# Kernel optimization log

Hardware: AMD Instinct MI355X
Metric: run time of the kernel (lower is better)

Reference implementation:

```python
import jax, jax.numpy as jnp
import numpy as np

B, T, D, H = 8, 2048, 1024, 128  # batch, seq, input_size, head_size


def setup_inputs() -> dict:
    key = jax.random.key(0)
    kx, kq, kk, kv = jax.random.split(key, 4)
    s = 1.0 / np.sqrt(D)
    return {
        "x": jax.random.normal(kx, (B, T, D), dtype=jnp.float32),
        "Wq": jax.random.normal(kq, (D, H), dtype=jnp.float32) * s,
        "Wk": jax.random.normal(kk, (D, H), dtype=jnp.float32) * s,
        "Wv": jax.random.normal(kv, (D, H), dtype=jnp.float32) * s,
    }


def reference(x, Wq, Wk, Wv):
    # projections (Linear, no bias)
    q = jnp.einsum("btd,dh->bth", x, Wq)
    k = jnp.einsum("btd,dh->bth", x, Wk)
    v = jnp.einsum("btd,dh->bth", x, Wv)
    scale = H ** (-0.5)
    scores = jnp.einsum("bth,bsh->bts", q, k) * scale  # [B,T,T]
    t = x.shape[1]
    causal = jnp.tril(jnp.ones((t, t), dtype=bool))
    scores = jnp.where(causal, scores, -jnp.inf)
    attn = jax.nn.softmax(scores, axis=-1)  # dropout p=0.0 -> identity
    out = jnp.einsum("bts,bsh->bth", attn, v)
    return out
```

## Files before the change

### kernel.cpp

```cpp
#include <hip/hip_runtime.h>
#include <math.h>

#define B_ 8
#define T_ 2048
#define D_ 1024
#define H_ 128
#define BT (B_ * T_)

typedef short bf16x8 __attribute__((ext_vector_type(8)));
typedef float f32x4 __attribute__((ext_vector_type(4)));

static constexpr float SCALE = 0.08838834764831845f;

__device__ inline unsigned short f2b(float f) {
  unsigned int u = __float_as_uint(f);
  u += 0x7FFF + ((u >> 16) & 1);
  return (unsigned short)(u >> 16);
}
__device__ inline unsigned int pk2(float a, float b) {
  return (unsigned int)f2b(a) | ((unsigned int)f2b(b) << 16);
}

__device__ __forceinline__ void gll16(const void* g, void* l) {
  __builtin_amdgcn_global_load_lds(
      (const __attribute__((address_space(1))) void*)g,
      (__attribute__((address_space(3))) void*)l, 16, 0, 0);
}

__global__ __launch_bounds__(256) void wcvt_kernel(
    const float* __restrict__ Wq, const float* __restrict__ Wk,
    const float* __restrict__ Wv, short* __restrict__ Wt) {
  __shared__ short Wls[128 * 72];
  const int sel = blockIdx.y;
  const float* W = sel == 0 ? Wq : (sel == 1 ? Wk : Wv);
  const int d0 = blockIdx.x * 64;
  const int tid = threadIdx.x;
#pragma unroll
  for (int i = 0; i < 8; ++i) {
    int slot = tid + i * 256;
    int r = slot >> 5, hg = slot & 31;
    float4 w = *(const float4*)(W + (size_t)(d0 + r) * H_ + hg * 4);
    Wls[(hg * 4 + 0) * 72 + r] = (short)f2b(w.x);
    Wls[(hg * 4 + 1) * 72 + r] = (short)f2b(w.y);
    Wls[(hg * 4 + 2) * 72 + r] = (short)f2b(w.z);
    Wls[(hg * 4 + 3) * 72 + r] = (short)f2b(w.w);
  }
  __syncthreads();
  short* dst = Wt + (size_t)sel * D_ * H_;
#pragma unroll
  for (int i = 0; i < 4; ++i) {
    int slot = tid + i * 256;
    int h = slot >> 3, g = slot & 7;
    *(int4*)(dst + (size_t)h * D_ + d0 + g * 8) = *(int4*)&Wls[h * 72 + g * 8];
  }
}

__global__ __launch_bounds__(256) void proj_kernel(
    const float* __restrict__ x, const short* __restrict__ Wt,
    short* __restrict__ qb, short* __restrict__ kb, short* __restrict__ vtb) {
  __shared__ alignas(16) char smem[49152];
  short* Xs0 = (short*)smem;
  short* Xs1 = (short*)(smem + 8192);
  short* Ws0 = (short*)(smem + 16384);
  short* Ws1 = (short*)(smem + 32768);

  const int tid = threadIdx.x;
  const int wave = tid >> 6, lane = tid & 63;
  const int ln = lane & 15, quad = lane >> 4;
  const int mw = wave & 1, nw = wave >> 1;
  const int sel = blockIdx.y;
  const int row0 = blockIdx.x * 64;
  const short* W = Wt + (size_t)sel * (size_t)(D_ * H_);

  f32x4 acc[2][4];
#pragma unroll
  for (int mi = 0; mi < 2; ++mi)
#pragma unroll
    for (int ni = 0; ni < 4; ++ni) acc[mi][ni] = (f32x4){0.f, 0.f, 0.f, 0.f};

  auto stage = [&](int bf, int k0) {
    short* Ws = bf ? Ws1 : Ws0;
#pragma unroll
    for (int j = 0; j < 4; ++j) {
      const int rbase = wave * 32 + j * 8;
      const int n = rbase + (lane >> 3);
      const int gp = (lane & 7) ^ (n & 7);
      gll16(W + (size_t)n * D_ + k0 + gp * 8, (char*)Ws + rbase * 128);
    }
    short* Xs = bf ? Xs1 : Xs0;
    float4 xr[4];
#pragma unroll
    for (int i = 0; i < 4; ++i) {
      int fid = tid + i * 256;
      int r = fid >> 4, g4 = fid & 15;
      xr[i] = *(const float4*)(x + (size_t)(row0 + r) * D_ + k0 + g4 * 4);
    }
#pragma unroll
    for (int i = 0; i < 4; ++i) {
      int fid = tid + i * 256;
      int r = fid >> 4, g4 = fid & 15;
      int g = g4 >> 1, half = g4 & 1;
      unsigned int* p = (unsigned int*)&Xs[r * 64 + ((g ^ (r & 7)) * 8) + half * 4];
      p[0] = pk2(xr[i].x, xr[i].y);
      p[1] = pk2(xr[i].z, xr[i].w);
    }
  };

  stage(0, 0);
  for (int s = 0; s < 16; ++s) {
    __syncthreads();
    if (s < 15) stage((s + 1) & 1, (s + 1) * 64);
    const short* Xs = (s & 1) ? Xs1 : Xs0;
    const short* Ws = (s & 1) ? Ws1 : Ws0;
#pragma unroll
    for (int kk = 0; kk < 2; ++kk) {
      bf16x8 a[2];
#pragma unroll
      for (int mi = 0; mi < 2; ++mi) {
        int r = mw * 32 + mi * 16 + ln;
        a[mi] = *(bf16x8*)&Xs[r * 64 + (((kk * 4 + quad) ^ (r & 7)) * 8)];
      }
#pragma unroll
      for (int ni = 0; ni < 4; ++ni) {
        int n = nw * 64 + ni * 16 + ln;
        bf16x8 bb = *(bf16x8*)&Ws[n * 64 + (((kk * 4 + quad) ^ (n & 7)) * 8)];
#pragma unroll
        for (int mi = 0; mi < 2; ++mi)
          acc[mi][ni] = __builtin_amdgcn_mfma_f32_16x16x32_bf16(a[mi], bb, acc[mi][ni], 0, 0, 0);
      }
    }
  }

  __syncthreads();
  short* Cs = (short*)smem;
  if (sel < 2) {
    short* out = sel ? kb : qb;
#pragma unroll
    for (int mi = 0; mi < 2; ++mi)
#pragma unroll
      for (int ni = 0; ni < 4; ++ni)
#pragma unroll
        for (int rr = 0; rr < 4; ++rr)
          Cs[(mw * 32 + mi * 16 + quad * 4 + rr) * 136 + nw * 64 + ni * 16 + ln] =
              (short)f2b(acc[mi][ni][rr]);
    __syncthreads();
#pragma unroll
    for (int i = 0; i < 4; ++i) {
      int slot = tid + i * 256;
      int r = slot >> 4, g = slot & 15;
      *(int4*)(out + (size_t)(row0 + r) * H_ + g * 8) = *(int4*)&Cs[r * 136 + g * 8];
    }
  } else {
#pragma unroll
    for (int mi = 0; mi < 2; ++mi)
#pragma unroll
      for (int ni = 0; ni < 4; ++ni)
#pragma unroll
        for (int rr = 0; rr < 4; ++rr)
          Cs[(nw * 64 + ni * 16 + ln) * 72 + mw * 32 + mi * 16 + quad * 4 + rr] =
              (short)f2b(acc[mi][ni][rr]);
    __syncthreads();
    const int b = row0 >> 11, t0 = row0 & 2047;
#pragma unroll
    for (int i = 0; i < 4; ++i) {
      int slot = tid + i * 256;
      int h = slot >> 3, g = slot & 7;
      *(int4*)(vtb + (size_t)(b * H_ + h) * T_ + t0 + g * 8) = *(int4*)&Cs[h * 72 + g * 8];
    }
  }
}

__global__ __launch_bounds__(256) void attn_part(
    const short* __restrict__ qb, const short* __restrict__ kb,
    const short* __restrict__ vtb, float* __restrict__ po,
    float* __restrict__ pm, float* __restrict__ pl) {
  __shared__ alignas(16) char smem[74240];
  short* Ks0 = (short*)smem;
  short* Ks1 = (short*)(smem + 16384);
  short* Vt0 = (short*)(smem + 32768);
  short* Vt1 = (short*)(smem + 49152);
  short* Pt  = (short*)(smem + 65536);

  const int tid = threadIdx.x;
  const int wv = tid >> 6, lane = tid & 63;
  const int ln = lane & 15, quad = lane >> 4;
  const int b = blockIdx.x / 80;
  const int rr = 79 - (blockIdx.x % 80);
  const int g = (rr >= 48) ? 3 : (rr >= 24) ? 2 : (rr >= 8) ? 1 : 0;
  const int local = rr - 4 * g * (g + 1);
  const int j = 8 * g + local / (g + 1);
  const int s = local - (local / (g + 1)) * (g + 1);
  const int sid = b * 80 + rr;
  const int q0 = j * 64;
  const int nchunks = min(8, j + 1 - 8 * s);

  short* myP = Pt + wv * (16 * 68);

  bf16x8 qfr[4];
#pragma unroll
  for (int kk = 0; kk < 4; ++kk)
    qfr[kk] = *(const bf16x8*)(qb + (size_t)(b * T_ + q0 + wv * 16 + ln) * H_ +
                               kk * 32 + quad * 8);

  f32x4 oacc[8];
#pragma unroll
  for (int ht = 0; ht < 8; ++ht) oacc[ht] = (f32x4){0.f, 0.f, 0.f, 0.f};

  float m_run = -INFINITY, l_run = 0.f;
  const int qglob = q0 + wv * 16 + ln;

  auto stageK = [&](short* dst, int s0) {
#pragma unroll
    for (int jj = 0; jj < 4; ++jj) {
      const int rb = wv * 16 + jj * 4;
      const int r = rb + (lane >> 4);
      const int gp = (lane & 15) ^ (r & 7);
      gll16(kb + (size_t)(b * T_ + s0 + r) * H_ + gp * 8, (char*)dst + rb * 256);
    }
  };
  auto stageV = [&](short* dst, int s0) {
#pragma unroll
    for (int jj = 0; jj < 4; ++jj) {
      const int hb = wv * 32 + jj * 8;
      const int h = hb + (lane >> 3);
      const int gp = (lane & 7) ^ (h & 7);
      gll16(vtb + (size_t)(b * H_ + h) * T_ + s0 + gp * 8, (char*)dst + hb * 128);
    }
  };

  stageK(Ks0, 8 * s * 64);
  stageV(Vt0, 8 * s * 64);

  for (int ch = 0; ch < nchunks; ++ch) {
    const int s0 = (8 * s + ch) * 64;
    const int cur = ch & 1;
    __syncthreads();
    if (ch + 1 < nchunks) {
      stageK(cur ? Ks0 : Ks1, s0 + 64);
      stageV(cur ? Vt0 : Vt1, s0 + 64);
    }
    const short* Kc = cur ? Ks1 : Ks0;
    const short* Vc = cur ? Vt1 : Vt0;

    f32x4 sacc[4];
#pragma unroll
    for (int t = 0; t < 4; ++t) sacc[t] = (f32x4){0.f, 0.f, 0.f, 0.f};
#pragma unroll
    for (int kk = 0; kk < 4; ++kk) {
#pragma unroll
      for (int t = 0; t < 4; ++t) {
        const int krow = t * 16 + ln;
        bf16x8 kf = *(bf16x8*)&Kc[krow * 128 + (((kk * 4 + quad) ^ (ln & 7)) * 8)];
        sacc[t] = __builtin_amdgcn_mfma_f32_16x16x32_bf16(kf, qfr[kk], sacc[t], 0, 0, 0);
      }
    }

    float sv[4][4];
    float mc = -INFINITY;
#pragma unroll
    for (int t = 0; t < 4; ++t)
#pragma unroll
      for (int r = 0; r < 4; ++r) {
        const int key = s0 + t * 16 + quad * 4 + r;
        float sc = sacc[t][r] * SCALE;
        sv[t][r] = (key <= qglob) ? sc : -INFINITY;
        mc = fmaxf(mc, sv[t][r]);
      }
    mc = fmaxf(mc, __shfl_xor(mc, 16));
    mc = fmaxf(mc, __shfl_xor(mc, 32));
    const float mnew = fmaxf(m_run, mc);
    const float alpha = __expf(m_run - mnew);
    float lc = 0.f;
    float p[4][4];
#pragma unroll
    for (int t = 0; t < 4; ++t)
#pragma unroll
      for (int r = 0; r < 4; ++r) {
        p[t][r] = __expf(sv[t][r] - mnew);
        lc += p[t][r];
      }
    lc += __shfl_xor(lc, 16);
    lc += __shfl_xor(lc, 32);
    l_run = l_run * alpha + lc;
    m_run = mnew;

#pragma unroll
    for (int t = 0; t < 4; ++t) {
      *(unsigned int*)&myP[ln * 68 + t * 16 + quad * 4 + 0] = pk2(p[t][0], p[t][1]);
      *(unsigned int*)&myP[ln * 68 + t * 16 + quad * 4 + 2] = pk2(p[t][2], p[t][3]);
    }
#pragma unroll
    for (int ht = 0; ht < 8; ++ht)
#pragma unroll
      for (int r = 0; r < 4; ++r) oacc[ht][r] *= alpha;

#pragma unroll
    for (int kk2 = 0; kk2 < 2; ++kk2) {
      bf16x8 pf = *(bf16x8*)&myP[ln * 68 + kk2 * 32 + quad * 8];
#pragma unroll
      for (int ht = 0; ht < 8; ++ht) {
        const int hrow = ht * 16 + ln;
        bf16x8 vf = *(bf16x8*)&Vc[hrow * 64 + (((kk2 * 4 + quad) ^ (ln & 7)) * 8)];
        oacc[ht] = __builtin_amdgcn_mfma_f32_16x16x32_bf16(vf, pf, oacc[ht], 0, 0, 0);
      }
    }
  }

  if (quad == 0) {
    pm[(size_t)sid * 64 + wv * 16 + ln] = m_run;
    pl[(size_t)sid * 64 + wv * 16 + ln] = l_run;
  }
  __syncthreads();
  float* Ot = (float*)smem;
#pragma unroll
  for (int ht = 0; ht < 8; ++ht)
    *(f32x4*)&Ot[(wv * 16 + ln) * 132 + ht * 16 + quad * 4] = oacc[ht];
  __syncthreads();
  float* dst = po + (size_t)sid * 8192;
#pragma unroll
  for (int i = 0; i < 8; ++i) {
    int slot2 = tid + i * 256;
    int r2 = slot2 >> 5, c2 = slot2 & 31;
    *(f32x4*)(dst + r2 * 128 + c2 * 4) = *(f32x4*)&Ot[r2 * 132 + c2 * 4];
  }
}

__global__ __launch_bounds__(256) void attn_reduce(
    const float* __restrict__ po, const float* __restrict__ pm,
    const float* __restrict__ pl, float* __restrict__ out) {
  const int b = blockIdx.x >> 5;
  const int j = blockIdx.x & 31;
  const int g = j >> 3;
  const int nseg = g + 1;
  const int sid0 = b * 80 + 4 * g * (g + 1) + (j - 8 * g) * nseg;
  const int tid = threadIdx.x;
  const int q = tid >> 2, hq = tid & 3;

  float m[4], l[4], a[4];
  float M = -INFINITY;
  for (int s2 = 0; s2 < nseg; ++s2) {
    m[s2] = pm[(size_t)(sid0 + s2) * 64 + q];
    l[s2] = pl[(size_t)(sid0 + s2) * 64 + q];
    M = fmaxf(M, m[s2]);
  }
  float lsum = 0.f;
  for (int s2 = 0; s2 < nseg; ++s2) {
    a[s2] = __expf(m[s2] - M);
    lsum += a[s2] * l[s2];
  }
  f32x4 acc[8];
#pragma unroll
  for (int i = 0; i < 8; ++i) acc[i] = (f32x4){0.f, 0.f, 0.f, 0.f};
  for (int s2 = 0; s2 < nseg; ++s2) {
    const float* src = po + (size_t)(sid0 + s2) * 8192 + q * 128 + hq * 32;
    const float as = a[s2];
#pragma unroll
    for (int i = 0; i < 8; ++i) {
      f32x4 v = *(const f32x4*)(src + i * 4);
#pragma unroll
      for (int c = 0; c < 4; ++c) acc[i][c] += as * v[c];
    }
  }
  const float inv = 1.0f / lsum;
  float* o = out + ((size_t)(b * T_ + j * 64 + q)) * H_ + hq * 32;
#pragma unroll
  for (int i = 0; i < 8; ++i) {
    f32x4 v;
#pragma unroll
    for (int c = 0; c < 4; ++c) v[c] = acc[i][c] * inv;
    *(f32x4*)(o + i * 4) = v;
  }
}

extern "C" void kernel_launch(void* const* d_in, const int* in_sizes, int n_in,
                              void* d_out, int out_size, void* d_ws, size_t ws_size,
                              hipStream_t stream) {
  const float* x  = (const float*)d_in[0];
  const float* Wq = (const float*)d_in[1];
  const float* Wk = (const float*)d_in[2];
  const float* Wv = (const float*)d_in[3];
  float* out = (float*)d_out;

  char* ws = (char*)d_ws;
  short* qb  = (short*)(ws);
  short* kb  = (short*)(ws + 4194304);
  short* vtb = (short*)(ws + 8388608);
  short* Wt  = (short*)(ws + 12582912);
  float* po  = (float*)(ws + 14680064);
  float* pm  = (float*)(ws + 35651584);
  float* pl  = (float*)(ws + 35915776);

  wcvt_kernel<<<dim3(D_ / 64, 3), 256, 0, stream>>>(Wq, Wk, Wv, Wt);
  proj_kernel<<<dim3(BT / 64, 3), 256, 0, stream>>>(x, Wt, qb, kb, vtb);
  attn_part<<<dim3(8 * 80), 256, 0, stream>>>(qb, kb, vtb, po, pm, pl);
  attn_reduce<<<dim3(8 * 32), 256, 0, stream>>>(po, pm, pl, out);
}
```

Before: 165.7 us.

## Enlarge attention query tile to 128 rows and overlap X loads with MFMA

The attention kernel now gives each wave 32 query rows (two 16-row sub-tiles) instead of 16. Each block covers 128 queries and the split-KV grid is halved, so each K/V chunk staged into LDS is reused twice as much. Score scaling is folded into a log2e-scaled constant so exp2f can be used, and the causal mask is applied only on chunks that cross the diagonal. The projection kernel issues the next X tile's global loads before the MFMA loop and packs them to LDS afterwards, hiding load latency. The cost is more registers per thread and fewer blocks (320), which may lower occupancy and load balance.

```diff
diff --git a/kernel.cpp b/kernel.cpp
--- a/kernel.cpp
+++ b/kernel.cpp
@@ -11,6 +11,7 @@
 typedef float f32x4 __attribute__((ext_vector_type(4)));
 
 static constexpr float SCALE = 0.08838834764831845f;
+static constexpr float SCALE2 = 0.127517416f;
 
 __device__ inline unsigned short f2b(float f) {
   unsigned int u = __float_as_uint(f);
@@ -78,7 +79,7 @@
 #pragma unroll
     for (int ni = 0; ni < 4; ++ni) acc[mi][ni] = (f32x4){0.f, 0.f, 0.f, 0.f};
 
-  auto stage = [&](int bf, int k0) {
+  auto stageW = [&](int bf, int k0) {
     short* Ws = bf ? Ws1 : Ws0;
 #pragma unroll
     for (int j = 0; j < 4; ++j) {
@@ -87,14 +88,9 @@
       const int gp = (lane & 7) ^ (n & 7);
       gll16(W + (size_t)n * D_ + k0 + gp * 8, (char*)Ws + rbase * 128);
     }
+  };
+  auto packX = [&](int bf, const float4* xr) {
     short* Xs = bf ? Xs1 : Xs0;
-    float4 xr[4];
-#pragma unroll
-    for (int i = 0; i < 4; ++i) {
-      int fid = tid + i * 256;
-      int r = fid >> 4, g4 = fid & 15;
-      xr[i] = *(const float4*)(x + (size_t)(row0 + r) * D_ + k0 + g4 * 4);
-    }
 #pragma unroll
     for (int i = 0; i < 4; ++i) {
       int fid = tid + i * 256;
@@ -106,10 +102,32 @@
     }
   };
 
-  stage(0, 0);
+  {
+    stageW(0, 0);
+    float4 xr[4];
+#pragma unroll
+    for (int i = 0; i < 4; ++i) {
+      int fid = tid + i * 256;
+      int r = fid >> 4, g4 = fid & 15;
+      xr[i] = *(const float4*)(x + (size_t)(row0 + r) * D_ + g4 * 4);
+    }
+    packX(0, xr);
+  }
+
   for (int s = 0; s < 16; ++s) {
     __syncthreads();
-    if (s < 15) stage((s + 1) & 1, (s + 1) * 64);
+    float4 xr[4];
+    const bool pre = (s < 15);
+    if (pre) {
+      const int k0n = (s + 1) * 64;
+      stageW((s + 1) & 1, k0n);
+#pragma unroll
+      for (int i = 0; i < 4; ++i) {
+        int fid = tid + i * 256;
+        int r = fid >> 4, g4 = fid & 15;
+        xr[i] = *(const float4*)(x + (size_t)(row0 + r) * D_ + k0n + g4 * 4);
+      }
+    }
     const short* Xs = (s & 1) ? Xs1 : Xs0;
     const short* Ws = (s & 1) ? Ws1 : Ws0;
 #pragma unroll
@@ -129,6 +147,7 @@
           acc[mi][ni] = __builtin_amdgcn_mfma_f32_16x16x32_bf16(a[mi], bb, acc[mi][ni], 0, 0, 0);
       }
     }
+    if (pre) packX((s + 1) & 1, xr);
   }
 
   __syncthreads();
@@ -184,30 +203,34 @@
   const int tid = threadIdx.x;
   const int wv = tid >> 6, lane = tid & 63;
   const int ln = lane & 15, quad = lane >> 4;
-  const int b = blockIdx.x / 80;
-  const int rr = 79 - (blockIdx.x % 80);
-  const int g = (rr >= 48) ? 3 : (rr >= 24) ? 2 : (rr >= 8) ? 1 : 0;
-  const int local = rr - 4 * g * (g + 1);
-  const int j = 8 * g + local / (g + 1);
-  const int s = local - (local / (g + 1)) * (g + 1);
-  const int sid = b * 80 + rr;
-  const int q0 = j * 64;
-  const int nchunks = min(8, j + 1 - 8 * s);
+  const int b = blockIdx.x / 40;
+  const int rr = 39 - (blockIdx.x % 40);
+  const int G = (rr >= 24) ? 3 : (rr >= 12) ? 2 : (rr >= 4) ? 1 : 0;
+  const int local = rr - 2 * G * (G + 1);
+  const int j = 4 * G + local / (G + 1);
+  const int s = local - (local / (G + 1)) * (G + 1);
+  const int sid = b * 40 + rr;
+  const int q0 = j * 128;
+  const int nchunks = min(8, 2 * j + 2 - 8 * s);
 
   short* myP = Pt + wv * (16 * 68);
 
-  bf16x8 qfr[4];
-#pragma unroll
-  for (int kk = 0; kk < 4; ++kk)
-    qfr[kk] = *(const bf16x8*)(qb + (size_t)(b * T_ + q0 + wv * 16 + ln) * H_ +
-                               kk * 32 + quad * 8);
-
-  f32x4 oacc[8];
-#pragma unroll
-  for (int ht = 0; ht < 8; ++ht) oacc[ht] = (f32x4){0.f, 0.f, 0.f, 0.f};
-
-  float m_run = -INFINITY, l_run = 0.f;
-  const int qglob = q0 + wv * 16 + ln;
+  bf16x8 qfr[2][4];
+#pragma unroll
+  for (int m = 0; m < 2; ++m)
+#pragma unroll
+    for (int kk = 0; kk < 4; ++kk)
+      qfr[m][kk] = *(const bf16x8*)(qb +
+          (size_t)(b * T_ + q0 + wv * 32 + m * 16 + ln) * H_ + kk * 32 + quad * 8);
+
+  f32x4 oacc[2][8];
+#pragma unroll
+  for (int m = 0; m < 2; ++m)
+#pragma unroll
+    for (int ht = 0; ht < 8; ++ht) oacc[m][ht] = (f32x4){0.f, 0.f, 0.f, 0.f};
+
+  float m_run[2] = {-INFINITY, -INFINITY};
+  float l_run[2] = {0.f, 0.f};
 
   auto stageK = [&](short* dst, int s0) {
 #pragma unroll
@@ -242,83 +265,102 @@
     const short* Kc = cur ? Ks1 : Ks0;
     const short* Vc = cur ? Vt1 : Vt0;
 
-    f32x4 sacc[4];
-#pragma unroll
-    for (int t = 0; t < 4; ++t) sacc[t] = (f32x4){0.f, 0.f, 0.f, 0.f};
+    f32x4 sacc[2][4];
+#pragma unroll
+    for (int m = 0; m < 2; ++m)
+#pragma unroll
+      for (int t = 0; t < 4; ++t) sacc[m][t] = (f32x4){0.f, 0.f, 0.f, 0.f};
 #pragma unroll
     for (int kk = 0; kk < 4; ++kk) {
 #pragma unroll
       for (int t = 0; t < 4; ++t) {
         const int krow = t * 16 + ln;
         bf16x8 kf = *(bf16x8*)&Kc[krow * 128 + (((kk * 4 + quad) ^ (ln & 7)) * 8)];
-        sacc[t] = __builtin_amdgcn_mfma_f32_16x16x32_bf16(kf, qfr[kk], sacc[t], 0, 0, 0);
-      }
-    }
-
-    float sv[4][4];
-    float mc = -INFINITY;
-#pragma unroll
-    for (int t = 0; t < 4; ++t)
-#pragma unroll
-      for (int r = 0; r < 4; ++r) {
-        const int key = s0 + t * 16 + quad * 4 + r;
-        float sc = sacc[t][r] * SCALE;
-        sv[t][r] = (key <= qglob) ? sc : -INFINITY;
-        mc = fmaxf(mc, sv[t][r]);
-      }
-    mc = fmaxf(mc, __shfl_xor(mc, 16));
-    mc = fmaxf(mc, __shfl_xor(mc, 32));
-    const float mnew = fmaxf(m_run, mc);
-    const float alpha = __expf(m_run - mnew);
-    float lc = 0.f;
-    float p[4][4];
-#pragma unroll
-    for (int t = 0; t < 4; ++t)
-#pragma unroll
-      for (int r = 0; r < 4; ++r) {
-        p[t][r] = __expf(sv[t][r] - mnew);
-        lc += p[t][r];
-      }
-    lc += __shfl_xor(lc, 16);
-    lc += __shfl_xor(lc, 32);
-    l_run = l_run * alpha + lc;
-    m_run = mnew;
-
-#pragma unroll
-    for (int t = 0; t < 4; ++t) {
-      *(unsigned int*)&myP[ln * 68 + t * 16 + quad * 4 + 0] = pk2(p[t][0], p[t][1]);
-      *(unsigned int*)&myP[ln * 68 + t * 16 + quad * 4 + 2] = pk2(p[t][2], p[t][3]);
-    }
-#pragma unroll
-    for (int ht = 0; ht < 8; ++ht)
-#pragma unroll
-      for (int r = 0; r < 4; ++r) oacc[ht][r] *= alpha;
-
-#pragma unroll
-    for (int kk2 = 0; kk2 < 2; ++kk2) {
-      bf16x8 pf = *(bf16x8*)&myP[ln * 68 + kk2 * 32 + quad * 8];
-#pragma unroll
-      for (int ht = 0; ht < 8; ++ht) {
-        const int hrow = ht * 16 + ln;
-        bf16x8 vf = *(bf16x8*)&Vc[hrow * 64 + (((kk2 * 4 + quad) ^ (ln & 7)) * 8)];
-        oacc[ht] = __builtin_amdgcn_mfma_f32_16x16x32_bf16(vf, pf, oacc[ht], 0, 0, 0);
+#pragma unroll
+        for (int m = 0; m < 2; ++m)
+          sacc[m][t] = __builtin_amdgcn_mfma_f32_16x16x32_bf16(kf, qfr[m][kk], sacc[m][t], 0, 0, 0);
+      }
+    }
+
+    const bool needMask = (s0 + 63 > q0 + wv * 32);
+    float p[2][4][4], alpha[2];
+#pragma unroll
+    for (int m = 0; m < 2; ++m) {
+      const int qg = q0 + wv * 32 + m * 16 + ln;
+      float sv[4][4];
+      float mc = -INFINITY;
+#pragma unroll
+      for (int t = 0; t < 4; ++t)
+#pragma unroll
+        for (int r = 0; r < 4; ++r) {
+          float scv = sacc[m][t][r] * SCALE2;
+          if (needMask) {
+            const int key = s0 + t * 16 + quad * 4 + r;
+            scv = (key <= qg) ? scv : -INFINITY;
+          }
+          sv[t][r] = scv;
+          mc = fmaxf(mc, scv);
+        }
+      mc = fmaxf(mc, __shfl_xor(mc, 16));
+      mc = fmaxf(mc, __shfl_xor(mc, 32));
+      const float mnew = fmaxf(m_run[m], mc);
+      alpha[m] = exp2f(m_run[m] - mnew);
+      float lc = 0.f;
+#pragma unroll
+      for (int t = 0; t < 4; ++t)
+#pragma unroll
+        for (int r = 0; r < 4; ++r) {
+          p[m][t][r] = exp2f(sv[t][r] - mnew);
+          lc += p[m][t][r];
+        }
+      lc += __shfl_xor(lc, 16);
+      lc += __shfl_xor(lc, 32);
+      l_run[m] = l_run[m] * alpha[m] + lc;
+      m_run[m] = mnew;
+    }
+
+#pragma unroll
+    for (int m = 0; m < 2; ++m) {
+#pragma unroll
+      for (int ht = 0; ht < 8; ++ht)
+#pragma unroll
+        for (int r = 0; r < 4; ++r) oacc[m][ht][r] *= alpha[m];
+#pragma unroll
+      for (int t = 0; t < 4; ++t) {
+        *(unsigned int*)&myP[ln * 68 + t * 16 + quad * 4 + 0] = pk2(p[m][t][0], p[m][t][1]);
+        *(unsigned int*)&myP[ln * 68 + t * 16 + quad * 4 + 2] = pk2(p[m][t][2], p[m][t][3]);
+      }
+#pragma unroll
+      for (int kk2 = 0; kk2 < 2; ++kk2) {
+        bf16x8 pf = *(bf16x8*)&myP[ln * 68 + kk2 * 32 + quad * 8];
+#pragma unroll
+        for (int ht = 0; ht < 8; ++ht) {
+          const int hrow = ht * 16 + ln;
+          bf16x8 vf = *(bf16x8*)&Vc[hrow * 64 + (((kk2 * 4 + quad) ^ (ln & 7)) * 8)];
+          oacc[m][ht] = __builtin_amdgcn_mfma_f32_16x16x32_bf16(vf, pf, oacc[m][ht], 0, 0, 0);
+        }
       }
     }
   }
 
   if (quad == 0) {
-    pm[(size_t)sid * 64 + wv * 16 + ln] = m_run;
-    pl[(size_t)sid * 64 + wv * 16 + ln] = l_run;
+#pragma unroll
+    for (int m = 0; m < 2; ++m) {
+      pm[(size_t)sid * 128 + wv * 32 + m * 16 + ln] = m_run[m];
+      pl[(size_t)sid * 128 + wv * 32 + m * 16 + ln] = l_run[m];
+    }
   }
   __syncthreads();
   float* Ot = (float*)smem;
 #pragma unroll
-  for (int ht = 0; ht < 8; ++ht)
-    *(f32x4*)&Ot[(wv * 16 + ln) * 132 + ht * 16 + quad * 4] = oacc[ht];
+  for (int m = 0; m < 2; ++m)
+#pragma unroll
+    for (int ht = 0; ht < 8; ++ht)
+      *(f32x4*)&Ot[(wv * 32 + m * 16 + ln) * 132 + ht * 16 + quad * 4] = oacc[m][ht];
   __syncthreads();
-  float* dst = po + (size_t)sid * 8192;
-#pragma unroll
-  for (int i = 0; i < 8; ++i) {
+  float* dst = po + (size_t)sid * 16384;
+#pragma unroll
+  for (int i = 0; i < 16; ++i) {
     int slot2 = tid + i * 256;
     int r2 = slot2 >> 5, c2 = slot2 & 31;
     *(f32x4*)(dst + r2 * 128 + c2 * 4) = *(f32x4*)&Ot[r2 * 132 + c2 * 4];
@@ -329,30 +371,31 @@
     const float* __restrict__ po, const float* __restrict__ pm,
     const float* __restrict__ pl, float* __restrict__ out) {
   const int b = blockIdx.x >> 5;
-  const int j = blockIdx.x & 31;
-  const int g = j >> 3;
-  const int nseg = g + 1;
-  const int sid0 = b * 80 + 4 * g * (g + 1) + (j - 8 * g) * nseg;
+  const int rem = blockIdx.x & 31;
+  const int j = rem >> 1, half = rem & 1;
+  const int G = j >> 2;
+  const int nseg = G + 1;
+  const int sid0 = b * 40 + 2 * G * (G + 1) + (j - 4 * G) * nseg;
   const int tid = threadIdx.x;
-  const int q = tid >> 2, hq = tid & 3;
-
-  float m[4], l[4], a[4];
-  float M = -INFINITY;
+  const int q = half * 64 + (tid >> 2), hq = tid & 3;
+
+  float m2[4], l[4], a[4];
+  float M2 = -INFINITY;
   for (int s2 = 0; s2 < nseg; ++s2) {
-    m[s2] = pm[(size_t)(sid0 + s2) * 64 + q];
-    l[s2] = pl[(size_t)(sid0 + s2) * 64 + q];
-    M = fmaxf(M, m[s2]);
+    m2[s2] = pm[(size_t)(sid0 + s2) * 128 + q];
+    l[s2] = pl[(size_t)(sid0 + s2) * 128 + q];
+    M2 = fmaxf(M2, m2[s2]);
   }
   float lsum = 0.f;
   for (int s2 = 0; s2 < nseg; ++s2) {
-    a[s2] = __expf(m[s2] - M);
+    a[s2] = exp2f(m2[s2] - M2);
     lsum += a[s2] * l[s2];
   }
   f32x4 acc[8];
 #pragma unroll
   for (int i = 0; i < 8; ++i) acc[i] = (f32x4){0.f, 0.f, 0.f, 0.f};
   for (int s2 = 0; s2 < nseg; ++s2) {
-    const float* src = po + (size_t)(sid0 + s2) * 8192 + q * 128 + hq * 32;
+    const float* src = po + (size_t)(sid0 + s2) * 16384 + q * 128 + hq * 32;
     const float as = a[s2];
 #pragma unroll
     for (int i = 0; i < 8; ++i) {
@@ -362,7 +405,7 @@
     }
   }
   const float inv = 1.0f / lsum;
-  float* o = out + ((size_t)(b * T_ + j * 64 + q)) * H_ + hq * 32;
+  float* o = out + ((size_t)(b * T_ + j * 128 + q)) * H_ + hq * 32;
 #pragma unroll
   for (int i = 0; i < 8; ++i) {
     f32x4 v;
@@ -392,6 +435,6 @@
 
   wcvt_kernel<<<dim3(D_ / 64, 3), 256, 0, stream>>>(Wq, Wk, Wv, Wt);
   proj_kernel<<<dim3(BT / 64, 3), 256, 0, stream>>>(x, Wt, qb, kb, vtb);
-  attn_part<<<dim3(8 * 80), 256, 0, stream>>>(qb, kb, vtb, po, pm, pl);
+  attn_part<<<dim3(8 * 40), 256, 0, stream>>>(qb, kb, vtb, po, pm, pl);
   attn_reduce<<<dim3(8 * 32), 256, 0, stream>>>(po, pm, pl, out);
 }
```

After: 172.7 us. 1.04x slower.

## Fuse Q/K/V projections into one block per row tile, loading weights directly

Applied to the files above, without the earlier changes.

The projection kernel now computes all three Q, K and V outputs (384 columns) in one block over 32-row tiles, rather than launching a separate grid slice per projection over 64-row tiles. Each fp32 x tile is read and converted to bf16 once instead of three times. The weight tiles no longer go through shared memory; each wave reads its B fragments straight from global memory (L2-resident) into registers. The trade-off is more register pressure (12 accumulators plus 12 weight fragments per wave), uncoalesced-ish per-lane weight loads sitting on the MFMA critical path, and a smaller grid.

```diff
diff --git a/kernel.cpp b/kernel.cpp
--- a/kernel.cpp
+++ b/kernel.cpp
@@ -58,45 +58,32 @@
 __global__ __launch_bounds__(256) void proj_kernel(
     const float* __restrict__ x, const short* __restrict__ Wt,
     short* __restrict__ qb, short* __restrict__ kb, short* __restrict__ vtb) {
-  __shared__ alignas(16) char smem[49152];
+  __shared__ alignas(16) char smem[27648];
   short* Xs0 = (short*)smem;
-  short* Xs1 = (short*)(smem + 8192);
-  short* Ws0 = (short*)(smem + 16384);
-  short* Ws1 = (short*)(smem + 32768);
+  short* Xs1 = (short*)(smem + 4096);
 
   const int tid = threadIdx.x;
   const int wave = tid >> 6, lane = tid & 63;
   const int ln = lane & 15, quad = lane >> 4;
-  const int mw = wave & 1, nw = wave >> 1;
-  const int sel = blockIdx.y;
-  const int row0 = blockIdx.x * 64;
-  const short* W = Wt + (size_t)sel * (size_t)(D_ * H_);
-
-  f32x4 acc[2][4];
+  const int row0 = blockIdx.x * 32;
+
+  f32x4 acc[2][6];
 #pragma unroll
   for (int mi = 0; mi < 2; ++mi)
 #pragma unroll
-    for (int ni = 0; ni < 4; ++ni) acc[mi][ni] = (f32x4){0.f, 0.f, 0.f, 0.f};
-
-  auto stage = [&](int bf, int k0) {
-    short* Ws = bf ? Ws1 : Ws0;
-#pragma unroll
-    for (int j = 0; j < 4; ++j) {
-      const int rbase = wave * 32 + j * 8;
-      const int n = rbase + (lane >> 3);
-      const int gp = (lane & 7) ^ (n & 7);
-      gll16(W + (size_t)n * D_ + k0 + gp * 8, (char*)Ws + rbase * 128);
-    }
+    for (int ni = 0; ni < 6; ++ni) acc[mi][ni] = (f32x4){0.f, 0.f, 0.f, 0.f};
+
+  const short* wp[6];
+#pragma unroll
+  for (int ni = 0; ni < 6; ++ni) {
+    int ng = wave * 96 + ni * 16 + ln;
+    wp[ni] = Wt + (size_t)(ng >> 7) * (D_ * H_) + (size_t)(ng & 127) * D_;
+  }
+
+  auto packX = [&](int bf, const float4* xr) {
     short* Xs = bf ? Xs1 : Xs0;
-    float4 xr[4];
-#pragma unroll
-    for (int i = 0; i < 4; ++i) {
-      int fid = tid + i * 256;
-      int r = fid >> 4, g4 = fid & 15;
-      xr[i] = *(const float4*)(x + (size_t)(row0 + r) * D_ + k0 + g4 * 4);
-    }
-#pragma unroll
-    for (int i = 0; i < 4; ++i) {
+#pragma unroll
+    for (int i = 0; i < 2; ++i) {
       int fid = tid + i * 256;
       int r = fid >> 4, g4 = fid & 15;
       int g = g4 >> 1, half = g4 & 1;
@@ -106,67 +93,87 @@
     }
   };
 
-  stage(0, 0);
+  {
+    float4 xr[2];
+#pragma unroll
+    for (int i = 0; i < 2; ++i) {
+      int fid = tid + i * 256;
+      int r = fid >> 4, g4 = fid & 15;
+      xr[i] = *(const float4*)(x + (size_t)(row0 + r) * D_ + g4 * 4);
+    }
+    packX(0, xr);
+  }
+
   for (int s = 0; s < 16; ++s) {
+    const int k0 = s * 64;
     __syncthreads();
-    if (s < 15) stage((s + 1) & 1, (s + 1) * 64);
+    float4 xr[2];
+    const bool pre = (s < 15);
+    if (pre) {
+      const int k0n = k0 + 64;
+#pragma unroll
+      for (int i = 0; i < 2; ++i) {
+        int fid = tid + i * 256;
+        int r = fid >> 4, g4 = fid & 15;
+        xr[i] = *(const float4*)(x + (size_t)(row0 + r) * D_ + k0n + g4 * 4);
+      }
+    }
+    bf16x8 wf[2][6];
+#pragma unroll
+    for (int kk = 0; kk < 2; ++kk)
+#pragma unroll
+      for (int ni = 0; ni < 6; ++ni)
+        wf[kk][ni] = *(const bf16x8*)(wp[ni] + k0 + kk * 32 + quad * 8);
+
     const short* Xs = (s & 1) ? Xs1 : Xs0;
-    const short* Ws = (s & 1) ? Ws1 : Ws0;
 #pragma unroll
     for (int kk = 0; kk < 2; ++kk) {
       bf16x8 a[2];
 #pragma unroll
       for (int mi = 0; mi < 2; ++mi) {
-        int r = mw * 32 + mi * 16 + ln;
+        int r = mi * 16 + ln;
         a[mi] = *(bf16x8*)&Xs[r * 64 + (((kk * 4 + quad) ^ (r & 7)) * 8)];
       }
 #pragma unroll
-      for (int ni = 0; ni < 4; ++ni) {
-        int n = nw * 64 + ni * 16 + ln;
-        bf16x8 bb = *(bf16x8*)&Ws[n * 64 + (((kk * 4 + quad) ^ (n & 7)) * 8)];
+      for (int ni = 0; ni < 6; ++ni)
 #pragma unroll
         for (int mi = 0; mi < 2; ++mi)
-          acc[mi][ni] = __builtin_amdgcn_mfma_f32_16x16x32_bf16(a[mi], bb, acc[mi][ni], 0, 0, 0);
-      }
-    }
+          acc[mi][ni] = __builtin_amdgcn_mfma_f32_16x16x32_bf16(a[mi], wf[kk][ni], acc[mi][ni], 0, 0, 0);
+    }
+    if (pre) packX((s + 1) & 1, xr);
   }
 
   __syncthreads();
-  short* Cs = (short*)smem;
-  if (sel < 2) {
-    short* out = sel ? kb : qb;
-#pragma unroll
-    for (int mi = 0; mi < 2; ++mi)
-#pragma unroll
-      for (int ni = 0; ni < 4; ++ni)
-#pragma unroll
-        for (int rr = 0; rr < 4; ++rr)
-          Cs[(mw * 32 + mi * 16 + quad * 4 + rr) * 136 + nw * 64 + ni * 16 + ln] =
-              (short)f2b(acc[mi][ni][rr]);
-    __syncthreads();
-#pragma unroll
-    for (int i = 0; i < 4; ++i) {
-      int slot = tid + i * 256;
-      int r = slot >> 4, g = slot & 15;
-      *(int4*)(out + (size_t)(row0 + r) * H_ + g * 8) = *(int4*)&Cs[r * 136 + g * 8];
-    }
-  } else {
-#pragma unroll
-    for (int mi = 0; mi < 2; ++mi)
-#pragma unroll
-      for (int ni = 0; ni < 4; ++ni)
-#pragma unroll
-        for (int rr = 0; rr < 4; ++rr)
-          Cs[(nw * 64 + ni * 16 + ln) * 72 + mw * 32 + mi * 16 + quad * 4 + rr] =
-              (short)f2b(acc[mi][ni][rr]);
-    __syncthreads();
-    const int b = row0 >> 11, t0 = row0 & 2047;
-#pragma unroll
-    for (int i = 0; i < 4; ++i) {
-      int slot = tid + i * 256;
-      int h = slot >> 3, g = slot & 7;
-      *(int4*)(vtb + (size_t)(b * H_ + h) * T_ + t0 + g * 8) = *(int4*)&Cs[h * 72 + g * 8];
-    }
+  short* CsQK = (short*)smem;
+  short* CsV  = (short*)(smem + 16896);
+#pragma unroll
+  for (int mi = 0; mi < 2; ++mi)
+#pragma unroll
+    for (int ni = 0; ni < 6; ++ni) {
+      int ng = wave * 96 + ni * 16 + ln;
+#pragma unroll
+      for (int rr = 0; rr < 4; ++rr) {
+        int row = mi * 16 + quad * 4 + rr;
+        float v = acc[mi][ni][rr];
+        if (ng < 256) CsQK[row * 264 + ng] = (short)f2b(v);
+        else          CsV[(ng - 256) * 40 + row] = (short)f2b(v);
+      }
+    }
+  __syncthreads();
+#pragma unroll
+  for (int i = 0; i < 4; ++i) {
+    int s2 = tid + i * 256;
+    int row = s2 >> 5, g = s2 & 31;
+    int4 v = *(int4*)&CsQK[row * 264 + g * 8];
+    if (g < 16) *(int4*)(qb + (size_t)(row0 + row) * H_ + g * 8) = v;
+    else        *(int4*)(kb + (size_t)(row0 + row) * H_ + (g - 16) * 8) = v;
+  }
+  const int b = row0 >> 11, t0 = row0 & 2047;
+#pragma unroll
+  for (int i = 0; i < 2; ++i) {
+    int s2 = tid + i * 256;
+    int h = s2 >> 2, g = s2 & 3;
+    *(int4*)(vtb + (size_t)(b * H_ + h) * T_ + t0 + g * 8) = *(int4*)&CsV[h * 40 + g * 8];
   }
 }
 
@@ -391,7 +398,7 @@
   float* pl  = (float*)(ws + 35915776);
 
   wcvt_kernel<<<dim3(D_ / 64, 3), 256, 0, stream>>>(Wq, Wk, Wv, Wt);
-  proj_kernel<<<dim3(BT / 64, 3), 256, 0, stream>>>(x, Wt, qb, kb, vtb);
+  proj_kernel<<<dim3(BT / 32), 256, 0, stream>>>(x, Wt, qb, kb, vtb);
   attn_part<<<dim3(8 * 80), 256, 0, stream>>>(qb, kb, vtb, po, pm, pl);
   attn_reduce<<<dim3(8 * 32), 256, 0, stream>>>(po, pm, pl, out);
 }
```

Result: slower. 194.6 us (+17.4%).
